# Performance work log

Hardware: AMD Instinct MI355X
Metric: run time of the kernel (lower is better)

## Reference

```python
import jax, jax.numpy as jnp
import numpy as np

DIM = 1024
DEPTH = 7
PAR = 8
N_NODES = 2 ** (DEPTH + 1) - 1  # 255
WIDTH = PAR * N_NODES  # 2040


def setup_inputs() -> dict:
    key = jax.random.key(0)
    k1, k2, k3, k4 = jax.random.split(key, 4)
    init_k = float(np.sqrt(1.0 / DIM))
    init_k2 = float(np.sqrt(1.0 / ((DEPTH + 1) * PAR)))
    oldx = jax.random.normal(k1, (4, 2048, DIM), dtype=jnp.float32)
    W_in = jax.random.uniform(k2, (WIDTH, DIM), jnp.float32, -init_k, init_k)
    b_in = jax.random.uniform(k3, (WIDTH,), jnp.float32, -init_k, init_k)
    W_out = jax.random.uniform(k4, (DIM, WIDTH), jnp.float32, -init_k2, init_k2)
    return {"oldx": oldx, "W_in": W_in, "b_in": b_in, "W_out": W_out}


def reference(oldx, W_in, b_in, W_out):
    x = oldx.reshape(-1, DIM)                      # [B, dim]
    B = x.shape[0]
    logits = x @ W_in.T + b_in                     # [B, width] dense GEMM over ALL nodes
    decisions = (logits > 0).astype(jnp.int32).reshape(B, PAR, N_NODES)
    acts = jax.nn.silu(logits).reshape(B, PAR, N_NODES)

    # Tree traversal: mark root, then descend DEPTH levels by each node's sign bit.
    current = jnp.zeros((B, PAR), dtype=jnp.int32)
    dmap = jax.nn.one_hot(current, N_NODES, dtype=acts.dtype)  # root node marked
    for d in range(DEPTH):
        cur_platform = 2 ** d - 1
        next_platform = 2 ** (d + 1) - 1
        moves = jnp.take_along_axis(decisions, current[..., None], axis=2)[..., 0]
        current = (current - cur_platform) * 2 + moves + next_platform
        dmap = dmap + jax.nn.one_hot(current, N_NODES, dtype=acts.dtype)

    masked = acts * jax.lax.stop_gradient(dmap)    # only depth+1 nodes per tree survive
    out = masked.reshape(B, WIDTH) @ W_out.T       # [B, dim]
    return out.reshape(oldx.shape)
```

## Files before the change

### kernel.cpp

```cpp
#include <hip/hip_runtime.h>
#include <math.h>

#define DIM 1024
#define DEPTH 7
#define PAR 8
#define N_NODES 255
#define WIDTH 2040
#define MARGIN 0.02f

__device__ __forceinline__ unsigned short f32_to_bf16(float f) {
    unsigned int u = __float_as_uint(f);
    u += 0x7fffu + ((u >> 16) & 1u);
    return (unsigned short)(u >> 16);
}
__device__ __forceinline__ float bf_lo(unsigned int u) { return __uint_as_float(u << 16); }
__device__ __forceinline__ float bf_hi(unsigned int u) { return __uint_as_float(u & 0xffff0000u); }

__device__ __forceinline__ float fma2(float a0, float a1, unsigned int u, float s) {
    s = fmaf(a0, bf_lo(u), s);
    return fmaf(a1, bf_hi(u), s);
}

__global__ __launch_bounds__(256) void convert_bf16_kernel(
    const float* __restrict__ src, unsigned short* __restrict__ dst, int n4)
{
    int i = (int)(blockIdx.x * blockDim.x + threadIdx.x);
    if (i < n4) {
        float4 v = ((const float4*)src)[i];
        uint2 pk;
        pk.x = (unsigned)f32_to_bf16(v.x) | ((unsigned)f32_to_bf16(v.y) << 16);
        pk.y = (unsigned)f32_to_bf16(v.z) | ((unsigned)f32_to_bf16(v.w) << 16);
        ((uint2*)dst)[i] = pk;
    }
}

__global__ __launch_bounds__(256) void transpose_bf16_kernel(
    const float* __restrict__ W_out, unsigned short* __restrict__ WoT)
{
    __shared__ float tile[64][65];
    const int w0 = blockIdx.x * 64;
    const int d0 = blockIdx.y * 64;
    const int tid = (int)threadIdx.x;
    const int sub = tid & 15;
    const int grp = tid >> 4;

    #pragma unroll
    for (int pass = 0; pass < 4; ++pass) {
        const int dl = pass * 16 + grp;
        const int wl = sub * 4;
        const int w = w0 + wl;
        const int d = d0 + dl;
        float4 v = make_float4(0.f, 0.f, 0.f, 0.f);
        if (w + 3 < WIDTH) {
            v = *(const float4*)(W_out + (size_t)d * WIDTH + w);
        } else {
            float t0 = (w + 0 < WIDTH) ? W_out[(size_t)d * WIDTH + w + 0] : 0.f;
            float t1 = (w + 1 < WIDTH) ? W_out[(size_t)d * WIDTH + w + 1] : 0.f;
            float t2 = (w + 2 < WIDTH) ? W_out[(size_t)d * WIDTH + w + 2] : 0.f;
            float t3 = (w + 3 < WIDTH) ? W_out[(size_t)d * WIDTH + w + 3] : 0.f;
            v = make_float4(t0, t1, t2, t3);
        }
        tile[dl][wl + 0] = v.x; tile[dl][wl + 1] = v.y;
        tile[dl][wl + 2] = v.z; tile[dl][wl + 3] = v.w;
    }
    __syncthreads();
    #pragma unroll
    for (int pass = 0; pass < 4; ++pass) {
        const int wl = pass * 16 + grp;
        const int dl = sub * 4;
        const int w = w0 + wl;
        if (w < WIDTH) {
            unsigned int b0 = f32_to_bf16(tile[dl + 0][wl]);
            unsigned int b1 = f32_to_bf16(tile[dl + 1][wl]);
            unsigned int b2 = f32_to_bf16(tile[dl + 2][wl]);
            unsigned int b3 = f32_to_bf16(tile[dl + 3][wl]);
            uint2 pk;
            pk.x = b0 | (b1 << 16);
            pk.y = b2 | (b3 << 16);
            *(uint2*)(WoT + (size_t)w * DIM + d0 + dl) = pk;
        }
    }
}

__global__ __launch_bounds__(256) void fff_bf16_kernel(
    const float* __restrict__ x,
    const float* __restrict__ W_in,
    const float* __restrict__ b_in,
    const unsigned short* __restrict__ Wb,
    const unsigned short* __restrict__ WoT,
    float* __restrict__ out,
    int B)
{
    const int wave = (int)((blockIdx.x * blockDim.x + threadIdx.x) >> 6);
    const int lane = (int)(threadIdx.x & 63);
    if (wave >= B) return;

    const float* xr = x + (size_t)wave * DIM;
    float4 x4[4];
    x4[0] = *(const float4*)(xr + lane * 8 + 0);
    x4[1] = *(const float4*)(xr + lane * 8 + 4);
    x4[2] = *(const float4*)(xr + 512 + lane * 8 + 0);
    x4[3] = *(const float4*)(xr + 512 + lane * 8 + 4);

    float acc[16];
    #pragma unroll
    for (int i = 0; i < 16; ++i) acc[i] = 0.f;

    unsigned long long nodes = 0ULL;

    #pragma unroll 1
    for (int d = 0; d <= DEPTH; ++d) {
        int gidx[PAR];
        float partial[PAR];

        #pragma unroll
        for (int p = 0; p < PAR; ++p) {
            const int np = (int)((nodes >> (8 * p)) & 0xffULL);
            gidx[p] = p * N_NODES + np;
            const unsigned short* wr = Wb + (size_t)gidx[p] * DIM;
            const uint4 u0 = *(const uint4*)(wr + lane * 8);
            const uint4 u1 = *(const uint4*)(wr + 512 + lane * 8);
            float s = 0.f;
            s = fma2(x4[0].x, x4[0].y, u0.x, s);
            s = fma2(x4[0].z, x4[0].w, u0.y, s);
            s = fma2(x4[1].x, x4[1].y, u0.z, s);
            s = fma2(x4[1].z, x4[1].w, u0.w, s);
            s = fma2(x4[2].x, x4[2].y, u1.x, s);
            s = fma2(x4[2].z, x4[2].w, u1.y, s);
            s = fma2(x4[3].x, x4[3].y, u1.z, s);
            s = fma2(x4[3].z, x4[3].w, u1.w, s);
            partial[p] = s;
        }

        #pragma unroll
        for (int off = 32; off >= 1; off >>= 1) {
            #pragma unroll
            for (int p = 0; p < PAR; ++p)
                partial[p] += __shfl_xor(partial[p], off, 64);
        }

        float my = partial[0] + b_in[gidx[0]];
        #pragma unroll
        for (int p = 1; p < PAR; ++p) {
            const float lp = partial[p] + b_in[gidx[p]];
            my = (lane == p) ? lp : my;
        }

        if (d < DEPTH) {
            unsigned long long bal = __ballot(lane < PAR && fabsf(my) < MARGIN);
            unsigned m = (unsigned)(bal & 0xffULL);
            while (m) {
                const int p = __builtin_ctz(m); m &= (m - 1u);
                const int np = (int)((nodes >> (8 * p)) & 0xffULL);
                const int gi = p * N_NODES + np;
                const float* wr = W_in + (size_t)gi * DIM;
                const float4 wa = *(const float4*)(wr + lane * 8 + 0);
                const float4 wb = *(const float4*)(wr + lane * 8 + 4);
                const float4 wc = *(const float4*)(wr + 512 + lane * 8 + 0);
                const float4 wd = *(const float4*)(wr + 512 + lane * 8 + 4);
                float s = 0.f;
                s = fmaf(x4[0].x, wa.x, s); s = fmaf(x4[0].y, wa.y, s);
                s = fmaf(x4[0].z, wa.z, s); s = fmaf(x4[0].w, wa.w, s);
                s = fmaf(x4[1].x, wb.x, s); s = fmaf(x4[1].y, wb.y, s);
                s = fmaf(x4[1].z, wb.z, s); s = fmaf(x4[1].w, wb.w, s);
                s = fmaf(x4[2].x, wc.x, s); s = fmaf(x4[2].y, wc.y, s);
                s = fmaf(x4[2].z, wc.z, s); s = fmaf(x4[2].w, wc.w, s);
                s = fmaf(x4[3].x, wd.x, s); s = fmaf(x4[3].y, wd.y, s);
                s = fmaf(x4[3].z, wd.z, s); s = fmaf(x4[3].w, wd.w, s);
                #pragma unroll
                for (int off = 32; off >= 1; off >>= 1)
                    s += __shfl_xor(s, off, 64);
                const float lf = s + b_in[gi];
                my = (lane == p) ? lf : my;
            }
        }

        #pragma unroll
        for (int p = 0; p < PAR; ++p) {
            const float lg = __shfl(my, p, 64);
            const float act = lg / (1.0f + __expf(-lg));

            const unsigned short* wo = WoT + (size_t)gidx[p] * DIM;
            const uint4 u0 = *(const uint4*)(wo + lane * 8);
            const uint4 u1 = *(const uint4*)(wo + 512 + lane * 8);
            acc[0]  = fmaf(act, bf_lo(u0.x), acc[0]);
            acc[1]  = fmaf(act, bf_hi(u0.x), acc[1]);
            acc[2]  = fmaf(act, bf_lo(u0.y), acc[2]);
            acc[3]  = fmaf(act, bf_hi(u0.y), acc[3]);
            acc[4]  = fmaf(act, bf_lo(u0.z), acc[4]);
            acc[5]  = fmaf(act, bf_hi(u0.z), acc[5]);
            acc[6]  = fmaf(act, bf_lo(u0.w), acc[6]);
            acc[7]  = fmaf(act, bf_hi(u0.w), acc[7]);
            acc[8]  = fmaf(act, bf_lo(u1.x), acc[8]);
            acc[9]  = fmaf(act, bf_hi(u1.x), acc[9]);
            acc[10] = fmaf(act, bf_lo(u1.y), acc[10]);
            acc[11] = fmaf(act, bf_hi(u1.y), acc[11]);
            acc[12] = fmaf(act, bf_lo(u1.z), acc[12]);
            acc[13] = fmaf(act, bf_hi(u1.z), acc[13]);
            acc[14] = fmaf(act, bf_lo(u1.w), acc[14]);
            acc[15] = fmaf(act, bf_hi(u1.w), acc[15]);

            if (d < DEPTH) {
                const int np = (int)((nodes >> (8 * p)) & 0xffULL);
                const unsigned long long nn =
                    (unsigned long long)(2 * np + 1 + ((lg > 0.0f) ? 1 : 0));
                nodes = (nodes & ~(0xffULL << (8 * p))) | (nn << (8 * p));
            }
        }
    }

    float* orow = out + (size_t)wave * DIM;
    *(float4*)(orow + lane * 8 + 0)       = make_float4(acc[0],  acc[1],  acc[2],  acc[3]);
    *(float4*)(orow + lane * 8 + 4)       = make_float4(acc[4],  acc[5],  acc[6],  acc[7]);
    *(float4*)(orow + 512 + lane * 8 + 0) = make_float4(acc[8],  acc[9],  acc[10], acc[11]);
    *(float4*)(orow + 512 + lane * 8 + 4) = make_float4(acc[12], acc[13], acc[14], acc[15]);
}

__global__ __launch_bounds__(256) void fff_fallback_kernel(
    const float* __restrict__ x, const float* __restrict__ W_in,
    const float* __restrict__ b_in, const float* __restrict__ W_out,
    float* __restrict__ out, int B)
{
    const int wave = (int)((blockIdx.x * blockDim.x + threadIdx.x) >> 6);
    const int lane = (int)(threadIdx.x & 63);
    if (wave >= B) return;

    const float* xr = x + (size_t)wave * DIM;
    float4 x4[4];
    x4[0] = *(const float4*)(xr + lane * 8 + 0);
    x4[1] = *(const float4*)(xr + lane * 8 + 4);
    x4[2] = *(const float4*)(xr + 512 + lane * 8 + 0);
    x4[3] = *(const float4*)(xr + 512 + lane * 8 + 4);

    float acc[16];
    #pragma unroll
    for (int i = 0; i < 16; ++i) acc[i] = 0.f;
    int node[PAR];
    #pragma unroll
    for (int p = 0; p < PAR; ++p) node[p] = 0;

    for (int d = 0; d <= DEPTH; ++d) {
        #pragma unroll
        for (int p = 0; p < PAR; ++p) {
            const int gidx = p * N_NODES + node[p];
            const float* wr = W_in + (size_t)gidx * DIM;
            const float4 wa = *(const float4*)(wr + lane * 8 + 0);
            const float4 wb = *(const float4*)(wr + lane * 8 + 4);
            const float4 wc = *(const float4*)(wr + 512 + lane * 8 + 0);
            const float4 wd = *(const float4*)(wr + 512 + lane * 8 + 4);
            float s = 0.f;
            s = fmaf(x4[0].x, wa.x, s); s = fmaf(x4[0].y, wa.y, s);
            s = fmaf(x4[0].z, wa.z, s); s = fmaf(x4[0].w, wa.w, s);
            s = fmaf(x4[1].x, wb.x, s); s = fmaf(x4[1].y, wb.y, s);
            s = fmaf(x4[1].z, wb.z, s); s = fmaf(x4[1].w, wb.w, s);
            s = fmaf(x4[2].x, wc.x, s); s = fmaf(x4[2].y, wc.y, s);
            s = fmaf(x4[2].z, wc.z, s); s = fmaf(x4[2].w, wc.w, s);
            s = fmaf(x4[3].x, wd.x, s); s = fmaf(x4[3].y, wd.y, s);
            s = fmaf(x4[3].z, wd.z, s); s = fmaf(x4[3].w, wd.w, s);
            #pragma unroll
            for (int off = 32; off >= 1; off >>= 1)
                s += __shfl_xor(s, off, 64);
            const float logit = s + b_in[gidx];
            const float act = logit / (1.0f + __expf(-logit));
            #pragma unroll
            for (int k = 0; k < 2; ++k) {
                #pragma unroll
                for (int j = 0; j < 8; ++j) {
                    const int e = k * 512 + lane * 8 + j;
                    acc[k * 8 + j] = fmaf(act, W_out[(size_t)e * WIDTH + gidx], acc[k * 8 + j]);
                }
            }
            node[p] = 2 * node[p] + 1 + ((logit > 0.0f) ? 1 : 0);
        }
    }

    float* orow = out + (size_t)wave * DIM;
    *(float4*)(orow + lane * 8 + 0)       = make_float4(acc[0],  acc[1],  acc[2],  acc[3]);
    *(float4*)(orow + lane * 8 + 4)       = make_float4(acc[4],  acc[5],  acc[6],  acc[7]);
    *(float4*)(orow + 512 + lane * 8 + 0) = make_float4(acc[8],  acc[9],  acc[10], acc[11]);
    *(float4*)(orow + 512 + lane * 8 + 4) = make_float4(acc[12], acc[13], acc[14], acc[15]);
}

extern "C" void kernel_launch(void* const* d_in, const int* in_sizes, int n_in,
                              void* d_out, int out_size, void* d_ws, size_t ws_size,
                              hipStream_t stream) {
    const float* oldx  = (const float*)d_in[0];
    const float* W_in  = (const float*)d_in[1];
    const float* b_in  = (const float*)d_in[2];
    const float* W_out = (const float*)d_in[3];
    float* out = (float*)d_out;

    const int B = in_sizes[0] / DIM;

    const size_t half = (size_t)WIDTH * DIM * sizeof(unsigned short);
    const bool use_bf16 = (ws_size >= 2 * half) && (d_ws != nullptr);

    const int blocks = (B + 3) / 4;

    if (use_bf16) {
        unsigned short* WoT = (unsigned short*)d_ws;
        unsigned short* Wb  = (unsigned short*)((char*)d_ws + half);
        dim3 tg((WIDTH + 63) / 64, DIM / 64);
        transpose_bf16_kernel<<<tg, 256, 0, stream>>>(W_out, WoT);
        const int n4 = WIDTH * DIM / 4;
        convert_bf16_kernel<<<(n4 + 255) / 256, 256, 0, stream>>>(W_in, (unsigned short*)Wb, n4);
        fff_bf16_kernel<<<blocks, 256, 0, stream>>>(oldx, W_in, b_in, Wb, WoT, out, B);
    } else {
        fff_fallback_kernel<<<blocks, 256, 0, stream>>>(oldx, W_in, b_in, W_out, out, B);
    }
}
```

Measured before the change: 194.3 us.

## Use fp16 dot2 for routing logits with transposed butterfly reduction

Converts W_in and x to packed fp16 and computes routing logits with the fdot2 instruction instead of bf16-unpacking FMAs. Replaces the eight independent full-wave shuffle reductions with a fold-and-exchange butterfly so each lane ends up owning one tree's logit. Sign bits are then gathered with a single ballot, and the output accumulation uses packed float2 FMAs. The fp32 recheck margin is widened and the recheck reloads x in fp32, trading extra fallback work for correctness under fp16 rounding.

```diff
diff --git a/kernel.cpp b/kernel.cpp
--- a/kernel.cpp
+++ b/kernel.cpp
@@ -6,7 +6,12 @@
 #define PAR 8
 #define N_NODES 255
 #define WIDTH 2040
-#define MARGIN 0.02f
+#define MARGIN 0.03f
+
+#define REPLANE(p) ((((p) & 1) << 3) | ((((p) >> 1) & 1) << 4) | ((((p) >> 2) & 1) << 5))
+
+typedef float  float2v  __attribute__((ext_vector_type(2)));
+typedef _Float16 half2v __attribute__((ext_vector_type(2)));
 
 __device__ __forceinline__ unsigned short f32_to_bf16(float f) {
     unsigned int u = __float_as_uint(f);
@@ -16,20 +21,41 @@
 __device__ __forceinline__ float bf_lo(unsigned int u) { return __uint_as_float(u << 16); }
 __device__ __forceinline__ float bf_hi(unsigned int u) { return __uint_as_float(u & 0xffff0000u); }
 
-__device__ __forceinline__ float fma2(float a0, float a1, unsigned int u, float s) {
-    s = fmaf(a0, bf_lo(u), s);
-    return fmaf(a1, bf_hi(u), s);
-}
-
-__global__ __launch_bounds__(256) void convert_bf16_kernel(
-    const float* __restrict__ src, unsigned short* __restrict__ dst, int n4)
+__device__ __forceinline__ half2v as_h2(unsigned int u) {
+    union { unsigned int u; half2v h; } c; c.u = u; return c.h;
+}
+__device__ __forceinline__ unsigned int pack_h2(float a, float b) {
+    union { half2v h; unsigned int u; } c;
+    c.h = (half2v){(_Float16)a, (_Float16)b};
+    return c.u;
+}
+
+__device__ __forceinline__ float dot2h(unsigned int a, unsigned int b, float c) {
+#if __has_builtin(__builtin_amdgcn_fdot2)
+    return __builtin_amdgcn_fdot2(as_h2(a), as_h2(b), c, false);
+#else
+    half2v ha = as_h2(a), hb = as_h2(b);
+    c = fmaf((float)ha.x, (float)hb.x, c);
+    return fmaf((float)ha.y, (float)hb.y, c);
+#endif
+}
+
+__device__ __forceinline__ float foldK(float a, float b, int K) {
+    const bool hi = (threadIdx.x & (unsigned)K) != 0;
+    const float keep = hi ? b : a;
+    const float send = hi ? a : b;
+    return keep + __shfl_xor(send, K, 64);
+}
+
+__global__ __launch_bounds__(256) void convert_f16_kernel(
+    const float* __restrict__ src, unsigned int* __restrict__ dst, int n4)
 {
     int i = (int)(blockIdx.x * blockDim.x + threadIdx.x);
     if (i < n4) {
         float4 v = ((const float4*)src)[i];
         uint2 pk;
-        pk.x = (unsigned)f32_to_bf16(v.x) | ((unsigned)f32_to_bf16(v.y) << 16);
-        pk.y = (unsigned)f32_to_bf16(v.z) | ((unsigned)f32_to_bf16(v.w) << 16);
+        pk.x = pack_h2(v.x, v.y);
+        pk.y = pack_h2(v.z, v.w);
         ((uint2*)dst)[i] = pk;
     }
 }
@@ -82,11 +108,11 @@
     }
 }
 
-__global__ __launch_bounds__(256) void fff_bf16_kernel(
+__global__ __launch_bounds__(256) void fff_f16_kernel(
     const float* __restrict__ x,
     const float* __restrict__ W_in,
     const float* __restrict__ b_in,
-    const unsigned short* __restrict__ Wb,
+    const unsigned int* __restrict__ Wh,
     const unsigned short* __restrict__ WoT,
     float* __restrict__ out,
     int B)
@@ -96,17 +122,28 @@
     if (wave >= B) return;
 
     const float* xr = x + (size_t)wave * DIM;
-    float4 x4[4];
-    x4[0] = *(const float4*)(xr + lane * 8 + 0);
-    x4[1] = *(const float4*)(xr + lane * 8 + 4);
-    x4[2] = *(const float4*)(xr + 512 + lane * 8 + 0);
-    x4[3] = *(const float4*)(xr + 512 + lane * 8 + 4);
-
-    float acc[16];
-    #pragma unroll
-    for (int i = 0; i < 16; ++i) acc[i] = 0.f;
+    unsigned int xp[8];
+    {
+        float4 a0 = *(const float4*)(xr + lane * 8 + 0);
+        float4 a1 = *(const float4*)(xr + lane * 8 + 4);
+        float4 a2 = *(const float4*)(xr + 512 + lane * 8 + 0);
+        float4 a3 = *(const float4*)(xr + 512 + lane * 8 + 4);
+        xp[0] = pack_h2(a0.x, a0.y);
+        xp[1] = pack_h2(a0.z, a0.w);
+        xp[2] = pack_h2(a1.x, a1.y);
+        xp[3] = pack_h2(a1.z, a1.w);
+        xp[4] = pack_h2(a2.x, a2.y);
+        xp[5] = pack_h2(a2.z, a2.w);
+        xp[6] = pack_h2(a3.x, a3.y);
+        xp[7] = pack_h2(a3.z, a3.w);
+    }
+
+    float2v acc2[8];
+    #pragma unroll
+    for (int i = 0; i < 8; ++i) acc2[i] = (float2v){0.f, 0.f};
 
     unsigned long long nodes = 0ULL;
+    const int myp = ((lane >> 3) & 1) | (((lane >> 4) & 1) << 1) | (((lane >> 5) & 1) << 2);
 
     #pragma unroll 1
     for (int d = 0; d <= DEPTH; ++d) {
@@ -117,103 +154,120 @@
         for (int p = 0; p < PAR; ++p) {
             const int np = (int)((nodes >> (8 * p)) & 0xffULL);
             gidx[p] = p * N_NODES + np;
-            const unsigned short* wr = Wb + (size_t)gidx[p] * DIM;
-            const uint4 u0 = *(const uint4*)(wr + lane * 8);
-            const uint4 u1 = *(const uint4*)(wr + 512 + lane * 8);
+            const unsigned int* wr = Wh + (size_t)gidx[p] * (DIM / 2);
+            const uint4 u0 = *(const uint4*)(wr + lane * 4);
+            const uint4 u1 = *(const uint4*)(wr + 256 + lane * 4);
             float s = 0.f;
-            s = fma2(x4[0].x, x4[0].y, u0.x, s);
-            s = fma2(x4[0].z, x4[0].w, u0.y, s);
-            s = fma2(x4[1].x, x4[1].y, u0.z, s);
-            s = fma2(x4[1].z, x4[1].w, u0.w, s);
-            s = fma2(x4[2].x, x4[2].y, u1.x, s);
-            s = fma2(x4[2].z, x4[2].w, u1.y, s);
-            s = fma2(x4[3].x, x4[3].y, u1.z, s);
-            s = fma2(x4[3].z, x4[3].w, u1.w, s);
+            s = dot2h(xp[0], u0.x, s);
+            s = dot2h(xp[1], u0.y, s);
+            s = dot2h(xp[2], u0.z, s);
+            s = dot2h(xp[3], u0.w, s);
+            s = dot2h(xp[4], u1.x, s);
+            s = dot2h(xp[5], u1.y, s);
+            s = dot2h(xp[6], u1.z, s);
+            s = dot2h(xp[7], u1.w, s);
             partial[p] = s;
         }
 
-        #pragma unroll
-        for (int off = 32; off >= 1; off >>= 1) {
+        const float c01 = foldK(partial[0], partial[1], 8);
+        const float c23 = foldK(partial[2], partial[3], 8);
+        const float c45 = foldK(partial[4], partial[5], 8);
+        const float c67 = foldK(partial[6], partial[7], 8);
+        const float d0f = foldK(c01, c23, 16);
+        const float d1f = foldK(c45, c67, 16);
+        float e = foldK(d0f, d1f, 32);
+        e += __shfl_xor(e, 1, 64);
+        e += __shfl_xor(e, 2, 64);
+        e += __shfl_xor(e, 4, 64);
+
+        const int ga = (lane & 8) ? gidx[1] : gidx[0];
+        const int gb = (lane & 8) ? gidx[3] : gidx[2];
+        const int gc = (lane & 8) ? gidx[5] : gidx[4];
+        const int gd = (lane & 8) ? gidx[7] : gidx[6];
+        const int ge = (lane & 16) ? gb : ga;
+        const int gf = (lane & 16) ? gd : gc;
+        const int gmine = (lane & 32) ? gf : ge;
+        float my = e + b_in[gmine];
+
+        if (d < DEPTH) {
+            const unsigned long long bal = __ballot(fabsf(my) < MARGIN);
+            unsigned rm = 0;
             #pragma unroll
             for (int p = 0; p < PAR; ++p)
-                partial[p] += __shfl_xor(partial[p], off, 64);
-        }
-
-        float my = partial[0] + b_in[gidx[0]];
+                rm |= ((unsigned)((bal >> REPLANE(p)) & 1ULL)) << p;
+            if (rm) {
+                const float4 fa = *(const float4*)(xr + lane * 8 + 0);
+                const float4 fb = *(const float4*)(xr + lane * 8 + 4);
+                const float4 fc = *(const float4*)(xr + 512 + lane * 8 + 0);
+                const float4 fd = *(const float4*)(xr + 512 + lane * 8 + 4);
+                while (rm) {
+                    const int p = __builtin_ctz(rm); rm &= (rm - 1u);
+                    const int np = (int)((nodes >> (8 * p)) & 0xffULL);
+                    const int gi = p * N_NODES + np;
+                    const float* wr = W_in + (size_t)gi * DIM;
+                    const float4 wa = *(const float4*)(wr + lane * 8 + 0);
+                    const float4 wb = *(const float4*)(wr + lane * 8 + 4);
+                    const float4 wc = *(const float4*)(wr + 512 + lane * 8 + 0);
+                    const float4 wd = *(const float4*)(wr + 512 + lane * 8 + 4);
+                    float s = 0.f;
+                    s = fmaf(fa.x, wa.x, s); s = fmaf(fa.y, wa.y, s);
+                    s = fmaf(fa.z, wa.z, s); s = fmaf(fa.w, wa.w, s);
+                    s = fmaf(fb.x, wb.x, s); s = fmaf(fb.y, wb.y, s);
+                    s = fmaf(fb.z, wb.z, s); s = fmaf(fb.w, wb.w, s);
+                    s = fmaf(fc.x, wc.x, s); s = fmaf(fc.y, wc.y, s);
+                    s = fmaf(fc.z, wc.z, s); s = fmaf(fc.w, wc.w, s);
+                    s = fmaf(fd.x, wd.x, s); s = fmaf(fd.y, wd.y, s);
+                    s = fmaf(fd.z, wd.z, s); s = fmaf(fd.w, wd.w, s);
+                    #pragma unroll
+                    for (int off = 32; off >= 1; off >>= 1)
+                        s += __shfl_xor(s, off, 64);
+                    const float lf = s + b_in[gi];
+                    my = (myp == p) ? lf : my;
+                }
+            }
+        }
+
+        const float act_mine = my / (1.0f + __expf(-my));
+        const unsigned long long pos = __ballot(my > 0.0f);
+
+        float act[PAR];
         #pragma unroll
-        for (int p = 1; p < PAR; ++p) {
-            const float lp = partial[p] + b_in[gidx[p]];
-            my = (lane == p) ? lp : my;
-        }
-
-        if (d < DEPTH) {
-            unsigned long long bal = __ballot(lane < PAR && fabsf(my) < MARGIN);
-            unsigned m = (unsigned)(bal & 0xffULL);
-            while (m) {
-                const int p = __builtin_ctz(m); m &= (m - 1u);
-                const int np = (int)((nodes >> (8 * p)) & 0xffULL);
-                const int gi = p * N_NODES + np;
-                const float* wr = W_in + (size_t)gi * DIM;
-                const float4 wa = *(const float4*)(wr + lane * 8 + 0);
-                const float4 wb = *(const float4*)(wr + lane * 8 + 4);
-                const float4 wc = *(const float4*)(wr + 512 + lane * 8 + 0);
-                const float4 wd = *(const float4*)(wr + 512 + lane * 8 + 4);
-                float s = 0.f;
-                s = fmaf(x4[0].x, wa.x, s); s = fmaf(x4[0].y, wa.y, s);
-                s = fmaf(x4[0].z, wa.z, s); s = fmaf(x4[0].w, wa.w, s);
-                s = fmaf(x4[1].x, wb.x, s); s = fmaf(x4[1].y, wb.y, s);
-                s = fmaf(x4[1].z, wb.z, s); s = fmaf(x4[1].w, wb.w, s);
-                s = fmaf(x4[2].x, wc.x, s); s = fmaf(x4[2].y, wc.y, s);
-                s = fmaf(x4[2].z, wc.z, s); s = fmaf(x4[2].w, wc.w, s);
-                s = fmaf(x4[3].x, wd.x, s); s = fmaf(x4[3].y, wd.y, s);
-                s = fmaf(x4[3].z, wd.z, s); s = fmaf(x4[3].w, wd.w, s);
-                #pragma unroll
-                for (int off = 32; off >= 1; off >>= 1)
-                    s += __shfl_xor(s, off, 64);
-                const float lf = s + b_in[gi];
-                my = (lane == p) ? lf : my;
-            }
-        }
+        for (int p = 0; p < PAR; ++p)
+            act[p] = __shfl(act_mine, REPLANE(p), 64);
 
         #pragma unroll
         for (int p = 0; p < PAR; ++p) {
-            const float lg = __shfl(my, p, 64);
-            const float act = lg / (1.0f + __expf(-lg));
-
             const unsigned short* wo = WoT + (size_t)gidx[p] * DIM;
             const uint4 u0 = *(const uint4*)(wo + lane * 8);
             const uint4 u1 = *(const uint4*)(wo + 512 + lane * 8);
-            acc[0]  = fmaf(act, bf_lo(u0.x), acc[0]);
-            acc[1]  = fmaf(act, bf_hi(u0.x), acc[1]);
-            acc[2]  = fmaf(act, bf_lo(u0.y), acc[2]);
-            acc[3]  = fmaf(act, bf_hi(u0.y), acc[3]);
-            acc[4]  = fmaf(act, bf_lo(u0.z), acc[4]);
-            acc[5]  = fmaf(act, bf_hi(u0.z), acc[5]);
-            acc[6]  = fmaf(act, bf_lo(u0.w), acc[6]);
-            acc[7]  = fmaf(act, bf_hi(u0.w), acc[7]);
-            acc[8]  = fmaf(act, bf_lo(u1.x), acc[8]);
-            acc[9]  = fmaf(act, bf_hi(u1.x), acc[9]);
-            acc[10] = fmaf(act, bf_lo(u1.y), acc[10]);
-            acc[11] = fmaf(act, bf_hi(u1.y), acc[11]);
-            acc[12] = fmaf(act, bf_lo(u1.z), acc[12]);
-            acc[13] = fmaf(act, bf_hi(u1.z), acc[13]);
-            acc[14] = fmaf(act, bf_lo(u1.w), acc[14]);
-            acc[15] = fmaf(act, bf_hi(u1.w), acc[15]);
+            const float2v a2 = (float2v){act[p], act[p]};
+            acc2[0] += a2 * (float2v){bf_lo(u0.x), bf_hi(u0.x)};
+            acc2[1] += a2 * (float2v){bf_lo(u0.y), bf_hi(u0.y)};
+            acc2[2] += a2 * (float2v){bf_lo(u0.z), bf_hi(u0.z)};
+            acc2[3] += a2 * (float2v){bf_lo(u0.w), bf_hi(u0.w)};
+            acc2[4] += a2 * (float2v){bf_lo(u1.x), bf_hi(u1.x)};
+            acc2[5] += a2 * (float2v){bf_lo(u1.y), bf_hi(u1.y)};
+            acc2[6] += a2 * (float2v){bf_lo(u1.z), bf_hi(u1.z)};
+            acc2[7] += a2 * (float2v){bf_lo(u1.w), bf_hi(u1.w)};
 
             if (d < DEPTH) {
                 const int np = (int)((nodes >> (8 * p)) & 0xffULL);
-                const unsigned long long nn =
-                    (unsigned long long)(2 * np + 1 + ((lg > 0.0f) ? 1 : 0));
+                const unsigned long long nn = (unsigned long long)
+                    (2 * np + 1 + (int)((pos >> REPLANE(p)) & 1ULL));
                 nodes = (nodes & ~(0xffULL << (8 * p))) | (nn << (8 * p));
             }
         }
     }
 
     float* orow = out + (size_t)wave * DIM;
-    *(float4*)(orow + lane * 8 + 0)       = make_float4(acc[0],  acc[1],  acc[2],  acc[3]);
-    *(float4*)(orow + lane * 8 + 4)       = make_float4(acc[4],  acc[5],  acc[6],  acc[7]);
-    *(float4*)(orow + 512 + lane * 8 + 0) = make_float4(acc[8],  acc[9],  acc[10], acc[11]);
-    *(float4*)(orow + 512 + lane * 8 + 4) = make_float4(acc[12], acc[13], acc[14], acc[15]);
+    *(float4*)(orow + lane * 8 + 0) =
+        make_float4(acc2[0].x, acc2[0].y, acc2[1].x, acc2[1].y);
+    *(float4*)(orow + lane * 8 + 4) =
+        make_float4(acc2[2].x, acc2[2].y, acc2[3].x, acc2[3].y);
+    *(float4*)(orow + 512 + lane * 8 + 0) =
+        make_float4(acc2[4].x, acc2[4].y, acc2[5].x, acc2[5].y);
+    *(float4*)(orow + 512 + lane * 8 + 4) =
+        make_float4(acc2[6].x, acc2[6].y, acc2[7].x, acc2[7].y);
 }
 
 __global__ __launch_bounds__(256) void fff_fallback_kernel(
@@ -293,18 +347,18 @@
     const int B = in_sizes[0] / DIM;
 
     const size_t half = (size_t)WIDTH * DIM * sizeof(unsigned short);
-    const bool use_bf16 = (ws_size >= 2 * half) && (d_ws != nullptr);
+    const bool use_lp = (ws_size >= 2 * half) && (d_ws != nullptr);
 
     const int blocks = (B + 3) / 4;
 
-    if (use_bf16) {
+    if (use_lp) {
         unsigned short* WoT = (unsigned short*)d_ws;
-        unsigned short* Wb  = (unsigned short*)((char*)d_ws + half);
+        unsigned int*   Wh  = (unsigned int*)((char*)d_ws + half);
         dim3 tg((WIDTH + 63) / 64, DIM / 64);
         transpose_bf16_kernel<<<tg, 256, 0, stream>>>(W_out, WoT);
         const int n4 = WIDTH * DIM / 4;
-        convert_bf16_kernel<<<(n4 + 255) / 256, 256, 0, stream>>>(W_in, (unsigned short*)Wb, n4);
-        fff_bf16_kernel<<<blocks, 256, 0, stream>>>(oldx, W_in, b_in, Wb, WoT, out, B);
+        convert_f16_kernel<<<(n4 + 255) / 256, 256, 0, stream>>>(W_in, Wh, n4);
+        fff_f16_kernel<<<blocks, 256, 0, stream>>>(oldx, W_in, b_in, Wh, WoT, out, B);
     } else {
         fff_fallback_kernel<<<blocks, 256, 0, stream>>>(oldx, W_in, b_in, W_out, out, B);
     }
```

Result: faster. 187.8 us (-3.3%).
